# Optimization experiments

Measured on AMD Instinct MI355X. Metric: run time of the kernel, lower is better.

Reference implementation:

```python
import jax, jax.numpy as jnp
import numpy as np

B, S, D = 8, 4096, 768
HEADS = 12
NEIGHBORS = 2
DILATION = 1
KERNEL = 1 + 2 * NEIGHBORS  # 5
DIM_HEAD = D // HEADS


def setup_inputs() -> dict:
    key = jax.random.key(0)
    ks = jax.random.split(key, 11)
    sc = 1.0 / np.sqrt(D)
    return {
        "x": jax.random.normal(ks[0], (B, S, D), dtype=jnp.float32),
        "Wq": jax.random.normal(ks[1], (D, D), dtype=jnp.float32) * sc,
        "bq": jax.random.normal(ks[2], (D,), dtype=jnp.float32) * 0.02,
        "Wk": jax.random.normal(ks[3], (D, D), dtype=jnp.float32) * sc,
        "bk": jax.random.normal(ks[4], (D,), dtype=jnp.float32) * 0.02,
        "Wv": jax.random.normal(ks[5], (D, D), dtype=jnp.float32) * sc,
        "bv": jax.random.normal(ks[6], (D,), dtype=jnp.float32) * 0.02,
        "Wo": jax.random.normal(ks[7], (D, D), dtype=jnp.float32) * sc,
        "bo": jax.random.normal(ks[8], (D,), dtype=jnp.float32) * 0.02,
        "gamma": jnp.ones((D,), dtype=jnp.float32),
        "beta": jnp.zeros((D,), dtype=jnp.float32),
    }


def _extract_seq_patches(x, kernel_size, dilation):
    # [B, S, D] -> [B, S, kernel_size, D] of dilated local windows, zero-padded.
    seq_len = x.shape[1]
    patch_size = kernel_size + (dilation - 1) * (kernel_size - 1)
    pad_r = (patch_size - 1) // 2
    pad_l = patch_size - pad_r - 1
    xp = jnp.pad(x, ((0, 0), (pad_l, pad_r), (0, 0)))
    # small fixed loop over kernel positions (kernel_size = 5)
    return jnp.stack([xp[:, i:i + seq_len] for i in range(0, patch_size, dilation)], axis=2)


def reference(x, Wq, bq, Wk, bk, Wv, bv, Wo, bo, gamma, beta):
    patches = _extract_seq_patches(x, KERNEL, DILATION)  # [B, S, K, D]
    q = x @ Wq + bq                                       # [B, S, D]
    k = patches @ Wk + bk                                 # [B, S, K, D]
    v = patches @ Wv + bv                                 # [B, S, K, D]
    # split heads
    q = q.reshape(B, S, HEADS, DIM_HEAD)
    k = k.reshape(B, S, KERNEL, HEADS, DIM_HEAD)
    v = v.reshape(B, S, KERNEL, HEADS, DIM_HEAD)
    scale = jnp.sqrt(jnp.asarray(DIM_HEAD, dtype=q.dtype))
    scores = jnp.einsum('bshd,bskhd->bshk', q, k) / scale  # [B, S, H, K]
    p = jax.nn.softmax(scores, axis=-1)
    att = jnp.einsum('bshk,bskhd->bshd', p, v)             # [B, S, H, dh]
    att = att.reshape(B, S, D)
    att = att @ Wo + bo
    y = att + x
    # LayerNorm over last dim
    mu = jnp.mean(y, axis=-1, keepdims=True)
    var = jnp.var(y, axis=-1, keepdims=True)
    y = (y - mu) / jnp.sqrt(var + 1e-5) * gamma + beta
    return y
```

## Files before the change

### kernel.cpp

```cpp
#include <hip/hip_runtime.h>

#define B_  8
#define S_  4096
#define D_  768
#define H_  12
#define M_  (B_ * S_)
#define NQKV_ 2304
#define NTILES 12

typedef unsigned short u16;
typedef __attribute__((ext_vector_type(4))) float  f32x4;
typedef __attribute__((ext_vector_type(8))) __bf16 bf16x8;
typedef __attribute__((ext_vector_type(4))) u16    u16x4;

#define GAS __attribute__((address_space(1)))
#define LAS __attribute__((address_space(3)))

__device__ __forceinline__ u16 f2bf(float f) {
    unsigned u = __float_as_uint(f);
    u += 0x7FFF + ((u >> 16) & 1);
    return (u16)(u >> 16);
}
__device__ __forceinline__ float bf2f(u16 h) {
    return __uint_as_float(((unsigned)h) << 16);
}

__device__ __forceinline__ void gload_lds16(const void* g, void* l) {
    __builtin_amdgcn_global_load_lds((const GAS void*)g, (LAS void*)l, 16, 0, 0);
}

__device__ __forceinline__ int xcd_swz(int bid, int nwg) {
    return (bid & 7) * (nwg >> 3) + (bid >> 3);
}

__global__ __launch_bounds__(256) void castx_kernel(const float* __restrict__ x,
                                                    u16* __restrict__ xb) {
    const int i = blockIdx.x * 256 + threadIdx.x;
    const float4 v = ((const float4*)x)[i];
    u16x4 o;
    o.x = f2bf(v.x); o.y = f2bf(v.y); o.z = f2bf(v.z); o.w = f2bf(v.w);
    ((u16x4*)xb)[i] = o;
}

__global__ __launch_bounds__(256) void wtrans_kernel(const float* __restrict__ Wq,
                                                     const float* __restrict__ Wk,
                                                     const float* __restrict__ Wv,
                                                     const float* __restrict__ Wo,
                                                     u16* __restrict__ Wb) {
    const float* W = (blockIdx.z == 0) ? Wq : (blockIdx.z == 1) ? Wk
                   : (blockIdx.z == 2) ? Wv : Wo;
    u16* O = Wb + (size_t)blockIdx.z * D_ * D_;
    __shared__ float tile[32][33];
    const int tx = threadIdx.x & 31, ty = threadIdx.x >> 5;
    const int k0 = blockIdx.y * 32, n0 = blockIdx.x * 32;
#pragma unroll
    for (int j = 0; j < 4; j++)
        tile[ty + j * 8][tx] = W[(size_t)(k0 + ty + j * 8) * D_ + n0 + tx];
    __syncthreads();
#pragma unroll
    for (int j = 0; j < 4; j++)
        O[(size_t)(n0 + ty + j * 8) * D_ + k0 + tx] = f2bf(tile[tx][ty + j * 8]);
}


#define PH_IN()                                              \
    __builtin_amdgcn_sched_barrier(0);                       \
    __builtin_amdgcn_s_barrier();                            \
    asm volatile("s_waitcnt lgkmcnt(0)" ::: "memory");       \
    __builtin_amdgcn_sched_barrier(0)

#define PH_OUT()                                             \
    __builtin_amdgcn_sched_barrier(0);                       \
    __builtin_amdgcn_s_barrier();                            \
    __builtin_amdgcn_sched_barrier(0)

#define PH_OUT_VM(N)                                         \
    __builtin_amdgcn_sched_barrier(0);                       \
    asm volatile("s_waitcnt vmcnt(" #N ")" ::: "memory");    \
    __builtin_amdgcn_s_barrier();                            \
    __builtin_amdgcn_sched_barrier(0)

#define MFMA_Q(AF, BF, MO, NO)                                               \
    __builtin_amdgcn_s_setprio(1);                                           \
    _Pragma("unroll") for (int mi = 0; mi < 4; ++mi)                         \
        _Pragma("unroll") for (int ni = 0; ni < 2; ++ni)                     \
            _Pragma("unroll") for (int kh = 0; kh < 2; ++kh)                 \
                acc[mi + MO][ni + NO] =                                      \
                    __builtin_amdgcn_mfma_f32_16x16x32_bf16(                 \
                        AF[mi][kh], BF[ni][kh], acc[mi + MO][ni + NO], 0, 0, 0); \
    __builtin_amdgcn_s_setprio(0)

#define RD(p, imm) (*(const bf16x8*)((p) + (imm)))

template <int MODE>
__global__ __launch_bounds__(512, 2) void gemm8_kernel(
    const u16* __restrict__ A, const u16* __restrict__ Wb,
    const float* __restrict__ b0, const float* __restrict__ b1,
    const float* __restrict__ b2,
    u16* __restrict__ outb, const u16* __restrict__ xres) {
    extern __shared__ char lds[];

    const int t = threadIdx.x;
    const int w = t >> 6, l = t & 63;
    const int wm = w >> 2, wn = w & 3;

    const int NTN = (MODE == 0) ? 9 : 3;
    const int work = xcd_swz(blockIdx.x, gridDim.x);
    const int mt = work / NTN, nt = work % NTN;
    const int m0 = mt * 256;
    const int n0 = nt * 256;
    const int widx = (MODE == 0) ? (n0 / D_) : 3;
    const int n0w = n0 - ((MODE == 0) ? widx * D_ : 0);

    const int srow   = t >> 3;
    const int schunk = (t & 7) ^ (srow & 7);
    const u16* Asrc = A + (size_t)(m0 + srow) * D_ + schunk * 8;
    const u16* Bsrc = Wb + (size_t)widx * (D_ * D_) + (size_t)(n0w + srow) * D_ + schunk * 8;

    auto STAGE_A = [&](int h, int tk, int db) {
        const u16* s = Asrc + (size_t)(h * 128) * D_ + tk * 64;
        char* d = lds + db * 65536 + h * 16384 + (w << 10);
        gload_lds16(s, d);
        gload_lds16(s + 64 * D_, d + 8192);
    };
    auto STAGE_B = [&](int h, int tk, int db) {
        const u16* s = Bsrc + (size_t)(h * 128) * D_ + tk * 64;
        char* d = lds + db * 65536 + 32768 + h * 16384 + (w << 10);
        gload_lds16(s, d);
        gload_lds16(s + 64 * D_, d + 8192);
    };

    const int ck0 = (((l >> 4) ^ (l & 7)) << 4);
    const int ck1 = ((((l >> 4) + 4) ^ (l & 7)) << 4);
    const int aRowB = (wm * 128 + (l & 15)) * 128;
    const int bRowB = 32768 + (wn * 64 + (l & 15)) * 128;
    const char* aC0[2] = { lds + aRowB + ck0, lds + 65536 + aRowB + ck0 };
    const char* aC1[2] = { lds + aRowB + ck1, lds + 65536 + aRowB + ck1 };
    const char* bC0[2] = { lds + bRowB + ck0, lds + 65536 + bRowB + ck0 };
    const char* bC1[2] = { lds + bRowB + ck1, lds + 65536 + bRowB + ck1 };

    f32x4 acc[8][4];
#pragma unroll
    for (int i = 0; i < 8; i++)
#pragma unroll
        for (int j = 0; j < 4; j++) acc[i][j] = (f32x4){0.f, 0.f, 0.f, 0.f};

    bf16x8 Alo[4][2], Ahi[4][2], Ba[2][2], Bb[2][2];

    STAGE_A(0, 0, 0); STAGE_A(1, 0, 0); STAGE_B(0, 0, 0); STAGE_B(1, 0, 0);
    STAGE_B(0, 1, 1); STAGE_B(1, 1, 1);
    __builtin_amdgcn_sched_barrier(0);
    asm volatile("s_waitcnt vmcnt(4)" ::: "memory");
    __builtin_amdgcn_s_barrier();
    __builtin_amdgcn_sched_barrier(0);

#pragma unroll
    for (int X = 0; X < NTILES; ++X) {
        const int c = X & 1;
        const int o = c ^ 1;
        const int t1 = (X + 1 < NTILES) ? X + 1 : X + 1 - NTILES;
        const int t2 = (X + 2 < NTILES) ? X + 2 : X + 2 - NTILES;

#pragma unroll
        for (int mi = 0; mi < 4; ++mi) {
            Alo[mi][0] = RD(aC0[c], mi * 2048);
            Alo[mi][1] = RD(aC1[c], mi * 2048);
        }
#pragma unroll
        for (int ni = 0; ni < 2; ++ni) {
            Ba[ni][0] = RD(bC0[c], ni * 2048);
            Ba[ni][1] = RD(bC1[c], ni * 2048);
        }
        STAGE_A(0, t1, o);
        asm volatile("s_waitcnt lgkmcnt(8)" ::: "memory");
        PH_IN();
        MFMA_Q(Alo, Ba, 0, 0);
        PH_OUT();

#pragma unroll
        for (int ni = 0; ni < 2; ++ni) {
            Bb[ni][0] = RD(bC0[c], (ni + 2) * 2048);
            Bb[ni][1] = RD(bC1[c], (ni + 2) * 2048);
        }
        STAGE_A(1, t1, o);
        PH_IN();
        MFMA_Q(Alo, Bb, 0, 2);
        PH_OUT();

#pragma unroll
        for (int mi = 0; mi < 4; ++mi) {
            Ahi[mi][0] = RD(aC0[c], (mi + 4) * 2048);
            Ahi[mi][1] = RD(aC1[c], (mi + 4) * 2048);
        }
        STAGE_B(0, t2, c);
        PH_IN();
        MFMA_Q(Ahi, Ba, 4, 0);
        PH_OUT();

        STAGE_B(1, t2, c);
        PH_IN();
        MFMA_Q(Ahi, Bb, 4, 2);
        PH_OUT_VM(4);
    }

    asm volatile("s_waitcnt vmcnt(0)" ::: "memory");

    const int crow0 = m0 + wm * 128 + ((l >> 4) << 2);
    const int ccol0 = n0 + wn * 64 + (l & 15);
    if (MODE == 0) {
        const float* bias = (widx == 0) ? b0 : (widx == 1) ? b1 : b2;
        const int bcol0 = ccol0 - widx * D_;
#pragma unroll
        for (int mi = 0; mi < 8; ++mi)
#pragma unroll
            for (int ni = 0; ni < 4; ++ni) {
                const float bv = bias[bcol0 + ni * 16];
#pragma unroll
                for (int r = 0; r < 4; ++r)
                    outb[(size_t)(crow0 + mi * 16 + r) * NQKV_ + ccol0 + ni * 16] =
                        f2bf(acc[mi][ni][r] + bv);
            }
    } else {
#pragma unroll
        for (int mi = 0; mi < 8; ++mi)
#pragma unroll
            for (int ni = 0; ni < 4; ++ni) {
                const int col = ccol0 + ni * 16;
                const float bv = b0[col];
#pragma unroll
                for (int r = 0; r < 4; ++r) {
                    const size_t idx = (size_t)(crow0 + mi * 16 + r) * D_ + col;
                    outb[idx] = f2bf(acc[mi][ni][r] + bv + bf2f(xres[idx]));
                }
            }
    }
}

__global__ __launch_bounds__(256) void attn_kernel(const u16* __restrict__ QKV,
                                                   const float* __restrict__ bk,
                                                   const float* __restrict__ bv,
                                                   u16* __restrict__ att) {
    const int gw = xcd_swz(blockIdx.x, gridDim.x) * 4 + (threadIdx.x >> 6);
    const int l  = threadIdx.x & 63;
    const int hq = gw % 3;
    const int m  = gw / 3;
    const int s  = m & (S_ - 1);
    const int col = hq * 256 + l * 4;
    const u16* base = QKV + (size_t)m * NQKV_;

    const u16x4 qv = *(const u16x4*)(base + col);
    float qf[4];
#pragma unroll
    for (int j = 0; j < 4; j++) qf[j] = bf2f(qv[j]);

    float sc[5];
#pragma unroll
    for (int i = 0; i < 5; i++) {
        const int sp = s + i - 2;
        float p;
        if (sp >= 0 && sp < S_) {
            const u16x4 kv = *(const u16x4*)(base + (i - 2) * NQKV_ + D_ + col);
            p = qf[0] * bf2f(kv[0]) + qf[1] * bf2f(kv[1])
              + qf[2] * bf2f(kv[2]) + qf[3] * bf2f(kv[3]);
        } else {
            const float4 kb = *(const float4*)(bk + col);
            p = qf[0] * kb.x + qf[1] * kb.y + qf[2] * kb.z + qf[3] * kb.w;
        }
#pragma unroll
        for (int off = 1; off < 16; off <<= 1) p += __shfl_xor(p, off, 64);
        sc[i] = p * 0.125f;
    }
    float mx = sc[0];
#pragma unroll
    for (int i = 1; i < 5; i++) mx = fmaxf(mx, sc[i]);
    float e[5], sum = 0.f;
#pragma unroll
    for (int i = 0; i < 5; i++) { e[i] = __expf(sc[i] - mx); sum += e[i]; }
    const float inv = 1.f / sum;

    float o[4] = {0.f, 0.f, 0.f, 0.f};
#pragma unroll
    for (int i = 0; i < 5; i++) {
        const float wgt = e[i] * inv;
        const int sp = s + i - 2;
        if (sp >= 0 && sp < S_) {
            const u16x4 vv = *(const u16x4*)(base + (i - 2) * NQKV_ + 2 * D_ + col);
#pragma unroll
            for (int j = 0; j < 4; j++) o[j] += wgt * bf2f(vv[j]);
        } else {
            const float4 vb = *(const float4*)(bv + col);
            o[0] += wgt * vb.x; o[1] += wgt * vb.y;
            o[2] += wgt * vb.z; o[3] += wgt * vb.w;
        }
    }
    u16x4 ov;
#pragma unroll
    for (int j = 0; j < 4; j++) ov[j] = f2bf(o[j]);
    *(u16x4*)(att + (size_t)m * D_ + col) = ov;
}

__global__ __launch_bounds__(256) void ln_kernel(const u16* __restrict__ Yb,
                                                 const float* __restrict__ gamma,
                                                 const float* __restrict__ beta,
                                                 float* __restrict__ out) {
    const int row = blockIdx.x;
    const u16* r = Yb + (size_t)row * D_;
    const int t = threadIdx.x;
    const float v0 = bf2f(r[t]), v1 = bf2f(r[t + 256]), v2 = bf2f(r[t + 512]);
    float s  = v0 + v1 + v2;
    float s2 = v0 * v0 + v1 * v1 + v2 * v2;
#pragma unroll
    for (int off = 32; off > 0; off >>= 1) {
        s  += __shfl_xor(s,  off, 64);
        s2 += __shfl_xor(s2, off, 64);
    }
    __shared__ float red[8];
    const int w = t >> 6, l = t & 63;
    if (l == 0) { red[w] = s; red[4 + w] = s2; }
    __syncthreads();
    s  = red[0] + red[1] + red[2] + red[3];
    s2 = red[4] + red[5] + red[6] + red[7];
    const float mu  = s * (1.f / 768.f);
    const float var = s2 * (1.f / 768.f) - mu * mu;
    const float inv = rsqrtf(var + 1e-5f);
    float* o = out + (size_t)row * D_;
    o[t]       = (v0 - mu) * inv * gamma[t]       + beta[t];
    o[t + 256] = (v1 - mu) * inv * gamma[t + 256] + beta[t + 256];
    o[t + 512] = (v2 - mu) * inv * gamma[t + 512] + beta[t + 512];
}

extern "C" void kernel_launch(void* const* d_in, const int* in_sizes, int n_in,
                              void* d_out, int out_size, void* d_ws, size_t ws_size,
                              hipStream_t stream) {
    const float* x     = (const float*)d_in[0];
    const float* Wq    = (const float*)d_in[1];
    const float* bq    = (const float*)d_in[2];
    const float* Wk    = (const float*)d_in[3];
    const float* bk    = (const float*)d_in[4];
    const float* Wv    = (const float*)d_in[5];
    const float* bv    = (const float*)d_in[6];
    const float* Wo    = (const float*)d_in[7];
    const float* bo    = (const float*)d_in[8];
    const float* gamma = (const float*)d_in[9];
    const float* beta  = (const float*)d_in[10];

    char* ws = (char*)d_ws;
    u16*   Wb  = (u16*)ws;
    u16*   xb  = (u16*)(ws + 4718592);
    u16*   QKV = (u16*)(ws + 4718592 + 50331648);
    u16*   yb  = QKV;
    u16*   att = (u16*)d_out;

    (void)hipFuncSetAttribute(reinterpret_cast<const void*>(&gemm8_kernel<0>),
                              hipFuncAttributeMaxDynamicSharedMemorySize, 131072);
    (void)hipFuncSetAttribute(reinterpret_cast<const void*>(&gemm8_kernel<1>),
                              hipFuncAttributeMaxDynamicSharedMemorySize, 131072);

    castx_kernel<<<(M_ * D_) / (256 * 4), 256, 0, stream>>>(x, xb);
    wtrans_kernel<<<dim3(24, 24, 4), 256, 0, stream>>>(Wq, Wk, Wv, Wo, Wb);
    gemm8_kernel<0><<<(M_ / 256) * 9, 512, 131072, stream>>>(xb, Wb, bq, bk, bv,
                                                             QKV, nullptr);
    attn_kernel<<<(M_ * 3) / 4, 256, 0, stream>>>(QKV, bk, bv, att);
    gemm8_kernel<1><<<(M_ / 256) * 3, 512, 131072, stream>>>(att, Wb, bo, nullptr, nullptr,
                                                             yb, xb);
    ln_kernel<<<M_, 256, 0, stream>>>(yb, gamma, beta, (float*)d_out);
}
```

Before: 300.9 us.

## Shrink GEMM tiles to 128x128 with 4-wave blocks and 64KB LDS

Replaces the 256x256-tile, 8-wave GEMM with a 128x128-tile, 4-wave version. Per-block LDS drops to 64KB and the grid grows four times. Staging offsets, swizzles and fragment loads are reworked for the smaller tile. The aim is better occupancy and load balance across CUs, at the cost of less data reuse per block and more global traffic for A and B. The explicit lgkmcnt wait before the first phase is also removed.

```diff
diff --git a/kernel.cpp b/kernel.cpp
--- a/kernel.cpp
+++ b/kernel.cpp
@@ -82,7 +82,7 @@
 
 #define MFMA_Q(AF, BF, MO, NO)                                               \
     __builtin_amdgcn_s_setprio(1);                                           \
-    _Pragma("unroll") for (int mi = 0; mi < 4; ++mi)                         \
+    _Pragma("unroll") for (int mi = 0; mi < 2; ++mi)                         \
         _Pragma("unroll") for (int ni = 0; ni < 2; ++ni)                     \
             _Pragma("unroll") for (int kh = 0; kh < 2; ++kh)                 \
                 acc[mi + MO][ni + NO] =                                      \
@@ -93,7 +93,7 @@
 #define RD(p, imm) (*(const bf16x8*)((p) + (imm)))
 
 template <int MODE>
-__global__ __launch_bounds__(512, 2) void gemm8_kernel(
+__global__ __launch_bounds__(256, 2) void gemm4_kernel(
     const u16* __restrict__ A, const u16* __restrict__ Wb,
     const float* __restrict__ b0, const float* __restrict__ b1,
     const float* __restrict__ b2,
@@ -102,53 +102,53 @@
 
     const int t = threadIdx.x;
     const int w = t >> 6, l = t & 63;
-    const int wm = w >> 2, wn = w & 3;
-
-    const int NTN = (MODE == 0) ? 9 : 3;
+    const int wm = w >> 1, wn = w & 1;
+
+    const int NTN = (MODE == 0) ? 18 : 6;
     const int work = xcd_swz(blockIdx.x, gridDim.x);
     const int mt = work / NTN, nt = work % NTN;
-    const int m0 = mt * 256;
-    const int n0 = nt * 256;
-    const int widx = (MODE == 0) ? (n0 / D_) : 3;
-    const int n0w = n0 - ((MODE == 0) ? widx * D_ : 0);
-
-    const int srow   = t >> 3;
-    const int schunk = (t & 7) ^ (srow & 7);
-    const u16* Asrc = A + (size_t)(m0 + srow) * D_ + schunk * 8;
-    const u16* Bsrc = Wb + (size_t)widx * (D_ * D_) + (size_t)(n0w + srow) * D_ + schunk * 8;
-
-    auto STAGE_A = [&](int h, int tk, int db) {
-        const u16* s = Asrc + (size_t)(h * 128) * D_ + tk * 64;
-        char* d = lds + db * 65536 + h * 16384 + (w << 10);
+    const int m0 = mt * 128;
+    const int col0 = nt * 128;
+    const int widx = (MODE == 0) ? (nt / 6) : 3;
+    const int n0w  = (MODE == 0) ? (nt % 6) * 128 : col0;
+
+    const int lrow = l >> 3;
+    const int schunk = (l & 7) ^ lrow;
+    const u16* AsrcB = A + (size_t)(m0 + w * 16 + lrow) * D_ + schunk * 8;
+    const u16* BsrcB = Wb + (size_t)widx * (D_ * D_)
+                          + (size_t)(n0w + w * 16 + lrow) * D_ + schunk * 8;
+    char* const dstA = lds + w * 2048;
+    char* const dstB = lds + 16384 + w * 2048;
+
+    auto STAGE_A = [&](int h, int tk, int bo) {
+        const u16* s = AsrcB + (size_t)(h * 64) * D_ + tk * 64;
+        char* d = dstA + bo + h * 8192;
         gload_lds16(s, d);
-        gload_lds16(s + 64 * D_, d + 8192);
+        gload_lds16(s + 8 * D_, d + 1024);
     };
-    auto STAGE_B = [&](int h, int tk, int db) {
-        const u16* s = Bsrc + (size_t)(h * 128) * D_ + tk * 64;
-        char* d = lds + db * 65536 + 32768 + h * 16384 + (w << 10);
+    auto STAGE_B = [&](int h, int tk, int bo) {
+        const u16* s = BsrcB + (size_t)(h * 64) * D_ + tk * 64;
+        char* d = dstB + bo + h * 8192;
         gload_lds16(s, d);
-        gload_lds16(s + 64 * D_, d + 8192);
+        gload_lds16(s + 8 * D_, d + 1024);
     };
 
-    const int ck0 = (((l >> 4) ^ (l & 7)) << 4);
-    const int ck1 = ((((l >> 4) + 4) ^ (l & 7)) << 4);
-    const int aRowB = (wm * 128 + (l & 15)) * 128;
-    const int bRowB = 32768 + (wn * 64 + (l & 15)) * 128;
-    const char* aC0[2] = { lds + aRowB + ck0, lds + 65536 + aRowB + ck0 };
-    const char* aC1[2] = { lds + aRowB + ck1, lds + 65536 + aRowB + ck1 };
-    const char* bC0[2] = { lds + bRowB + ck0, lds + 65536 + bRowB + ck0 };
-    const char* bC1[2] = { lds + bRowB + ck1, lds + 65536 + bRowB + ck1 };
-
-    f32x4 acc[8][4];
-#pragma unroll
-    for (int i = 0; i < 8; i++)
+    const int fr = l & 15;
+    const int ck0 = (((l >> 4) ^ (fr & 7)) << 4);
+    const int ck1 = ((((l >> 4) + 4) ^ (fr & 7)) << 4);
+    const char* aB = lds + (wm * 64 + fr) * 128;
+    const char* bB = lds + 16384 + (wn * 64 + fr) * 128;
+
+    f32x4 acc[4][4];
+#pragma unroll
+    for (int i = 0; i < 4; i++)
 #pragma unroll
         for (int j = 0; j < 4; j++) acc[i][j] = (f32x4){0.f, 0.f, 0.f, 0.f};
 
-    bf16x8 Alo[4][2], Ahi[4][2], Ba[2][2], Bb[2][2];
+    bf16x8 Amlo[2][2], Amhi[2][2], Bnlo[2][2], Bnhi[2][2];
 
     STAGE_A(0, 0, 0); STAGE_A(1, 0, 0); STAGE_B(0, 0, 0); STAGE_B(1, 0, 0);
-    STAGE_B(0, 1, 1); STAGE_B(1, 1, 1);
+    STAGE_B(0, 1, 32768); STAGE_B(1, 1, 32768);
     __builtin_amdgcn_sched_barrier(0);
     asm volatile("s_waitcnt vmcnt(4)" ::: "memory");
     __builtin_amdgcn_s_barrier();
@@ -156,62 +156,60 @@
 
 #pragma unroll
     for (int X = 0; X < NTILES; ++X) {
-        const int c = X & 1;
-        const int o = c ^ 1;
+        const int cb = (X & 1) * 32768;
+        const int ob = cb ^ 32768;
         const int t1 = (X + 1 < NTILES) ? X + 1 : X + 1 - NTILES;
         const int t2 = (X + 2 < NTILES) ? X + 2 : X + 2 - NTILES;
 
 #pragma unroll
-        for (int mi = 0; mi < 4; ++mi) {
-            Alo[mi][0] = RD(aC0[c], mi * 2048);
-            Alo[mi][1] = RD(aC1[c], mi * 2048);
+        for (int mi = 0; mi < 2; ++mi) {
+            Amlo[mi][0] = RD(aB, cb + mi * 2048 + ck0);
+            Amlo[mi][1] = RD(aB, cb + mi * 2048 + ck1);
         }
 #pragma unroll
         for (int ni = 0; ni < 2; ++ni) {
-            Ba[ni][0] = RD(bC0[c], ni * 2048);
-            Ba[ni][1] = RD(bC1[c], ni * 2048);
-        }
-        STAGE_A(0, t1, o);
-        asm volatile("s_waitcnt lgkmcnt(8)" ::: "memory");
+            Bnlo[ni][0] = RD(bB, cb + ni * 2048 + ck0);
+            Bnlo[ni][1] = RD(bB, cb + ni * 2048 + ck1);
+        }
+        STAGE_A(0, t1, ob);
         PH_IN();
-        MFMA_Q(Alo, Ba, 0, 0);
+        MFMA_Q(Amlo, Bnlo, 0, 0);
         PH_OUT();
 
 #pragma unroll
         for (int ni = 0; ni < 2; ++ni) {
-            Bb[ni][0] = RD(bC0[c], (ni + 2) * 2048);
-            Bb[ni][1] = RD(bC1[c], (ni + 2) * 2048);
-        }
-        STAGE_A(1, t1, o);
+            Bnhi[ni][0] = RD(bB, cb + (ni + 2) * 2048 + ck0);
+            Bnhi[ni][1] = RD(bB, cb + (ni + 2) * 2048 + ck1);
+        }
+        STAGE_A(1, t1, ob);
         PH_IN();
-        MFMA_Q(Alo, Bb, 0, 2);
+        MFMA_Q(Amlo, Bnhi, 0, 2);
         PH_OUT();
 
 #pragma unroll
-        for (int mi = 0; mi < 4; ++mi) {
-            Ahi[mi][0] = RD(aC0[c], (mi + 4) * 2048);
-            Ahi[mi][1] = RD(aC1[c], (mi + 4) * 2048);
-        }
-        STAGE_B(0, t2, c);
+        for (int mi = 0; mi < 2; ++mi) {
+            Amhi[mi][0] = RD(aB, cb + (mi + 2) * 2048 + ck0);
+            Amhi[mi][1] = RD(aB, cb + (mi + 2) * 2048 + ck1);
+        }
+        STAGE_B(0, t2, cb);
         PH_IN();
-        MFMA_Q(Ahi, Ba, 4, 0);
+        MFMA_Q(Amhi, Bnlo, 2, 0);
         PH_OUT();
 
-        STAGE_B(1, t2, c);
+        STAGE_B(1, t2, cb);
         PH_IN();
-        MFMA_Q(Ahi, Bb, 4, 2);
+        MFMA_Q(Amhi, Bnhi, 2, 2);
         PH_OUT_VM(4);
     }
-
     asm volatile("s_waitcnt vmcnt(0)" ::: "memory");
 
-    const int crow0 = m0 + wm * 128 + ((l >> 4) << 2);
-    const int ccol0 = n0 + wn * 64 + (l & 15);
+    const int crow0 = m0 + wm * 64 + ((l >> 4) << 2);
+    const int ccol0 = col0 + wn * 64 + fr;
     if (MODE == 0) {
         const float* bias = (widx == 0) ? b0 : (widx == 1) ? b1 : b2;
         const int bcol0 = ccol0 - widx * D_;
 #pragma unroll
-        for (int mi = 0; mi < 8; ++mi)
+        for (int mi = 0; mi < 4; ++mi)
 #pragma unroll
             for (int ni = 0; ni < 4; ++ni) {
                 const float bv = bias[bcol0 + ni * 16];
@@ -222,7 +220,7 @@
             }
     } else {
 #pragma unroll
-        for (int mi = 0; mi < 8; ++mi)
+        for (int mi = 0; mi < 4; ++mi)
 #pragma unroll
             for (int ni = 0; ni < 4; ++ni) {
                 const int col = ccol0 + ni * 16;
@@ -351,17 +349,17 @@
     u16*   yb  = QKV;
     u16*   att = (u16*)d_out;
 
-    (void)hipFuncSetAttribute(reinterpret_cast<const void*>(&gemm8_kernel<0>),
-                              hipFuncAttributeMaxDynamicSharedMemorySize, 131072);
-    (void)hipFuncSetAttribute(reinterpret_cast<const void*>(&gemm8_kernel<1>),
-                              hipFuncAttributeMaxDynamicSharedMemorySize, 131072);
+    (void)hipFuncSetAttribute(reinterpret_cast<const void*>(&gemm4_kernel<0>),
+                              hipFuncAttributeMaxDynamicSharedMemorySize, 65536);
+    (void)hipFuncSetAttribute(reinterpret_cast<const void*>(&gemm4_kernel<1>),
+                              hipFuncAttributeMaxDynamicSharedMemorySize, 65536);
 
     castx_kernel<<<(M_ * D_) / (256 * 4), 256, 0, stream>>>(x, xb);
     wtrans_kernel<<<dim3(24, 24, 4), 256, 0, stream>>>(Wq, Wk, Wv, Wo, Wb);
-    gemm8_kernel<0><<<(M_ / 256) * 9, 512, 131072, stream>>>(xb, Wb, bq, bk, bv,
+    gemm4_kernel<0><<<(M_ / 128) * 18, 256, 65536, stream>>>(xb, Wb, bq, bk, bv,
                                                              QKV, nullptr);
     attn_kernel<<<(M_ * 3) / 4, 256, 0, stream>>>(QKV, bk, bv, att);
-    gemm8_kernel<1><<<(M_ / 256) * 3, 512, 131072, stream>>>(att, Wb, bo, nullptr, nullptr,
-                                                             yb, xb);
+    gemm4_kernel<1><<<(M_ / 128) * 6, 256, 65536, stream>>>(att, Wb, bo, nullptr, nullptr,
+                                                            yb, xb);
     ln_kernel<<<M_, 256, 0, stream>>>(yb, gamma, beta, (float*)d_out);
 }
```

Measured after the change: 297.8 us. About the same (-1.0%).
